# Kernel tuning notes

Measured on AMD Instinct MI355X. Metric: run time of the kernel, lower is better.

Reference implementation:

```python
import jax, jax.numpy as jnp
import numpy as np

NUM_MIRNA = 20000
NUM_GENE = 30000
N = NUM_MIRNA + NUM_GENE  # 50000 homogeneous nodes
R = 4                      # num_relations
E = 1000000                # num edges
IN_C, HID, OUT, NB = 128, 128, 64, 10


def setup_inputs() -> dict:
    key = jax.random.key(0)
    ks = jax.random.split(key, 20)
    s = 0.05
    inp = {}
    inp["x_mirna"] = jax.random.normal(ks[0], (NUM_MIRNA, 256), jnp.float32)
    inp["x_gene"] = jax.random.normal(ks[1], (NUM_GENE, 512), jnp.float32)
    inp["edge_index"] = jax.random.randint(ks[2], (2, E), 0, N)
    inp["edge_type"] = jax.random.randint(ks[3], (E,), 0, R)
    # per-node-type input projections
    inp["lin_w_m"] = jax.random.normal(ks[4], (256, IN_C), jnp.float32) * s
    inp["lin_b_m"] = jnp.zeros((IN_C,), jnp.float32)
    inp["lin_w_g"] = jax.random.normal(ks[5], (512, IN_C), jnp.float32) * s
    inp["lin_b_g"] = jnp.zeros((IN_C,), jnp.float32)
    # RGCNConv layer 1 (basis decomposition)
    inp["comp1"] = jax.random.normal(ks[6], (R, NB), jnp.float32) * s
    inp["basis1"] = jax.random.normal(ks[7], (NB, IN_C, HID), jnp.float32) * s
    inp["root1"] = jax.random.normal(ks[8], (IN_C, HID), jnp.float32) * s
    inp["bias1"] = jnp.zeros((HID,), jnp.float32)
    # RGCNConv layer 2
    inp["comp2"] = jax.random.normal(ks[9], (R, NB), jnp.float32) * s
    inp["basis2"] = jax.random.normal(ks[10], (NB, HID, OUT), jnp.float32) * s
    inp["root2"] = jax.random.normal(ks[11], (HID, OUT), jnp.float32) * s
    inp["bias2"] = jnp.zeros((OUT,), jnp.float32)
    return inp


def rgcn_conv(x, src, dst, etype, comp, basis, root, bias):
    # W_r = sum_b comp[r,b] * basis[b] : [R, I, O]
    W = jnp.einsum('rb,bio->rio', comp, basis)
    # transform every node under every relation: [R, N, O]
    h = jnp.einsum('ni,rio->rno', x, W)
    # gather per-edge message from (relation, source) pair: [E, O]
    msg = h[etype, src]
    # per-(relation, dst) mean aggregation (PyG RGCNConv aggr='mean')
    seg = etype * N + dst
    summed = jax.ops.segment_sum(msg, seg, num_segments=R * N)
    cnt = jax.ops.segment_sum(jnp.ones((msg.shape[0],), msg.dtype), seg,
                              num_segments=R * N)
    mean = summed / jnp.maximum(cnt, 1.0)[:, None]
    agg = mean.reshape(R, N, -1).sum(0)  # sum over relations
    return agg + x @ root + bias


def reference(x_mirna, x_gene, edge_index, edge_type,
              lin_w_m, lin_b_m, lin_w_g, lin_b_g,
              comp1, basis1, root1, bias1,
              comp2, basis2, root2, bias2):
    xm = x_mirna @ lin_w_m + lin_b_m
    xg = x_gene @ lin_w_g + lin_b_g
    x = jnp.concatenate([xm, xg], axis=0)  # to_homogeneous, miRNA first
    src, dst = edge_index[0], edge_index[1]
    x = rgcn_conv(x, src, dst, edge_type, comp1, basis1, root1, bias1)
    x = rgcn_conv(x, src, dst, edge_type, comp2, basis2, root2, bias2)
    return x[:NUM_MIRNA], x[NUM_MIRNA:]
```

## Files before the change

kernel.cpp:

```cpp
#include <hip/hip_runtime.h>
#include <hip/hip_bf16.h>

#define NUM_MIRNA 20000
#define NUM_GENE  30000
#define NN        50000
#define RR        4
#define EE        1000000
#define IN_C      128
#define HIDC      128
#define OUTC      64
#define NBASIS    10
#define NSEG      (RR * NN)
#define NSEGP     200704
#define KFUSE     640
#define SROW      512

#define NBKT   256
#define BSH    8
#define NBKTU  ((NN + 255) >> 8)
#define CHUNK  4096
#define NCHUNK ((EE + CHUNK - 1) / CHUNK)

typedef __attribute__((ext_vector_type(8))) short bf16x8;
typedef __attribute__((ext_vector_type(4))) float f32x4;
typedef __attribute__((ext_vector_type(2))) float f32x2;

__device__ inline ushort f2bf(float x) {
    uint u = __float_as_uint(x);
    uint r = u + 0x7fffu + ((u >> 16) & 1u);
    return (ushort)(r >> 16);
}
__device__ inline float bf2f(ushort b) {
    return __uint_as_float((uint)b << 16);
}
__device__ inline uint pack2bf(float lo, float hi) {
    return (uint)f2bf(lo) | ((uint)f2bf(hi) << 16);
}
__device__ inline f32x2 up2(uint u) {
    return (f32x2){__uint_as_float(u << 16), __uint_as_float(u & 0xffff0000u)};
}

#define GLOAD_LDS16(gsrc, ldst)                                                \
    __builtin_amdgcn_global_load_lds(                                          \
        (const __attribute__((address_space(1))) void*)(gsrc),                 \
        (__attribute__((address_space(3))) void*)(ldst), 16, 0, 0)

__global__ void cvt_k(const float* __restrict__ in, ushort* __restrict__ out, int n4) {
    int i = blockIdx.x * 256 + threadIdx.x;
    if (i >= n4) return;
    float4 v = ((const float4*)in)[i];
    ushort4 o;
    o.x = f2bf(v.x); o.y = f2bf(v.y); o.z = f2bf(v.z); o.w = f2bf(v.w);
    ((ushort4*)out)[i] = o;
}

__global__ void tcast_k(const float* __restrict__ W, ushort* __restrict__ Wt,
                        int K, int OC) {
    int idx = blockIdx.x * 256 + threadIdx.x;
    if (idx >= K * OC) return;
    int o = idx / K, k = idx % K;
    Wt[idx] = f2bf(W[(size_t)k * OC + o]);
}

__global__ void buildW_k(const float* __restrict__ comp, const float* __restrict__ basis,
                         const float* __restrict__ root, ushort* __restrict__ Wt, int O) {
    int idx = blockIdx.x * 256 + threadIdx.x;
    if (idx >= O * KFUSE) return;
    int o = idx / KFUSE, k = idx % KFUSE;
    float acc;
    if (k < 512) {
        int r = k >> 7, i = k & 127;
        acc = 0.f;
#pragma unroll
        for (int b = 0; b < NBASIS; ++b)
            acc += comp[r * NBASIS + b] * basis[((size_t)b * 128 + i) * O + o];
    } else {
        acc = root[(size_t)(k - 512) * O + o];
    }
    Wt[idx] = f2bf(acc);
}

template <int NT, int K, bool OUT_BF16, bool ROOTX>
__global__ __launch_bounds__(256) void sgemm_k(
    const ushort* __restrict__ A, const ushort* __restrict__ xroot,
    const ushort* __restrict__ Wt, const float* __restrict__ bias,
    void* __restrict__ Cout, int M)
{
    constexpr int OC = 2 * NT * 16;
    constexpr int BK = 64;
    constexpr int NTILE = K / BK;
    constexpr int AS = ROOTX ? SROW : K;

    __shared__ __align__(16) ushort As[2 * 4096];

    const int tid  = threadIdx.x;
    const int lane = tid & 63;
    const int wid  = tid >> 6;
    const int wm   = wid >> 1;
    const int wn   = wid & 1;
    const int l15  = lane & 15;
    const int lg   = lane >> 4;
    const int rowBase = blockIdx.x * 64;
    const int colBase = wn * NT * 16;

    f32x4 acc[2][NT];
#pragma unroll
    for (int mt = 0; mt < 2; ++mt)
#pragma unroll
        for (int nt = 0; nt < NT; ++nt)
            acc[mt][nt] = (f32x4){0.f, 0.f, 0.f, 0.f};

    auto STAGE = [&](int buf, int t) {
        const int kc = t * BK;
#pragma unroll
        for (int i = 0; i < 2; ++i) {
            int L   = i * 4096 + tid * 16;
            int row = L >> 7;
            int bs  = (L & 127) ^ ((row & 7) << 4);
            int grow = rowBase + row; if (grow >= M) grow = M - 1;
            const ushort* src;
            if (!ROOTX || kc < SROW)
                src = A + (size_t)grow * AS + kc + (bs >> 1);
            else
                src = xroot + (size_t)grow * IN_C + (kc - SROW) + (bs >> 1);
            GLOAD_LDS16(src, &As[(size_t)buf * 4096 + (L >> 1)]);
        }
    };

    STAGE(0, 0);
    __syncthreads();

#pragma unroll
    for (int t = 0; t < NTILE; ++t) {
        const int kc  = t * BK;
        const int buf = t & 1;

        bf16x8 bB[2][NT];
#pragma unroll
        for (int kk = 0; kk < 2; ++kk)
#pragma unroll
            for (int nt = 0; nt < NT; ++nt)
                bB[kk][nt] = *(const bf16x8*)(
                    Wt + (size_t)(colBase + nt * 16 + l15) * K + kc + kk * 32 + lg * 8);

        if (t + 1 < NTILE) STAGE(buf ^ 1, t + 1);

        bf16x8 aF[2][2];
#pragma unroll
        for (int mt = 0; mt < 2; ++mt)
#pragma unroll
            for (int kk = 0; kk < 2; ++kk) {
                int row = wm * 32 + mt * 16 + l15;
                int kb  = kk * 64 + lg * 16;
                aF[mt][kk] = *(const bf16x8*)&As[
                    (size_t)buf * 4096 + row * 64 + ((kb ^ ((row & 7) << 4)) >> 1)];
            }

#pragma unroll
        for (int kk = 0; kk < 2; ++kk)
#pragma unroll
            for (int nt = 0; nt < NT; ++nt)
#pragma unroll
                for (int mt = 0; mt < 2; ++mt)
                    acc[mt][nt] = __builtin_amdgcn_mfma_f32_16x16x32_bf16(
                        aF[mt][kk], bB[kk][nt], acc[mt][nt], 0, 0, 0);

        __syncthreads();
    }

#pragma unroll
    for (int nt = 0; nt < NT; ++nt) {
        int n = colBase + nt * 16 + l15;
        float bv = bias ? bias[n] : 0.f;
#pragma unroll
        for (int mt = 0; mt < 2; ++mt) {
#pragma unroll
            for (int q = 0; q < 4; ++q) {
                int m = rowBase + wm * 32 + mt * 16 + lg * 4 + q;
                if (m < M) {
                    float v = acc[mt][nt][q] + bv;
                    size_t off = (size_t)m * OC + n;
                    if (OUT_BF16) ((ushort*)Cout)[off] = f2bf(v);
                    else          ((float*)Cout)[off]  = v;
                }
            }
        }
    }
}

__global__ __launch_bounds__(256) void bs0_k(const int* __restrict__ dstA,
                                             int* __restrict__ bcnt) {
    __shared__ int h[NBKT];
    int t = threadIdx.x;
    h[t] = 0;
    __syncthreads();
    int e0 = blockIdx.x * CHUNK;
    int n = EE - e0; if (n > CHUNK) n = CHUNK;
    for (int i = t; i < n; i += 256)
        atomicAdd(&h[dstA[e0 + i] >> BSH], 1);
    __syncthreads();
    if (h[t]) atomicAdd(&bcnt[t], h[t]);
}

__global__ void bscan_k(const int* __restrict__ bcnt, int* __restrict__ bbase,
                        int* __restrict__ bcur) {
    __shared__ int sm[NBKT];
    int t = threadIdx.x;
    int v = bcnt[t];
    sm[t] = v; __syncthreads();
    for (int off = 1; off < NBKT; off <<= 1) {
        int x = (t >= off) ? sm[t - off] : 0;
        __syncthreads();
        sm[t] += x;
        __syncthreads();
    }
    int ex = sm[t] - v;
    bbase[t] = ex;
    bcur[t]  = ex;
}

__global__ __launch_bounds__(256) void bs1_k(const int* __restrict__ srcA,
                                             const int* __restrict__ dstA,
                                             const int* __restrict__ et,
                                             int* __restrict__ bcur,
                                             uint2* __restrict__ bpay) {
    __shared__ int h[NBKT], cur[NBKT], boff[NBKT];
    __shared__ int lseg[CHUNK];
    __shared__ int lsrc[CHUNK];
    int t = threadIdx.x;
    h[t] = 0; cur[t] = 0;
    __syncthreads();
    int e0 = blockIdx.x * CHUNK;
    int n = EE - e0; if (n > CHUNK) n = CHUNK;
    for (int i = t; i < n; i += 256) {
        int e = e0 + i;
        int d = dstA[e];
        int s2 = d * 4 + et[e];
        lseg[i] = s2;
        lsrc[i] = srcA[e];
        atomicAdd(&h[d >> BSH], 1);
    }
    __syncthreads();
    if (h[t]) boff[t] = atomicAdd(&bcur[t], h[t]);
    __syncthreads();
    for (int i = t; i < n; i += 256) {
        int s2 = lseg[i];
        int b = s2 >> (BSH + 2);
        int slot = atomicAdd(&cur[b], 1);
        bpay[boff[b] + slot] = make_uint2((uint)lsrc[i], (uint)s2);
    }
}

__global__ __launch_bounds__(256) void sortbkt_k(
    const uint2* __restrict__ bpay, const int* __restrict__ bbase,
    const int* __restrict__ bcnt, int* __restrict__ sorted,
    int* __restrict__ cnt, int* __restrict__ base, float* __restrict__ inv)
{
    __shared__ int hist[1024];
    __shared__ int tsum[256];
    const int b = blockIdx.x;
    const int t = threadIdx.x;
    const int segbase = b << 10;

#pragma unroll
    for (int i = 0; i < 4; ++i) hist[t + i * 256] = 0;
    __syncthreads();

    const int e0 = bbase[b];
    const int n  = bcnt[b];
    for (int i = t; i < n; i += 256)
        atomicAdd(&hist[(int)bpay[e0 + i].y - segbase], 1);
    __syncthreads();

    int h0 = hist[t * 4], h1 = hist[t * 4 + 1], h2 = hist[t * 4 + 2], h3 = hist[t * 4 + 3];
    int s = h0 + h1 + h2 + h3;
    tsum[t] = s; __syncthreads();
    for (int off = 1; off < 256; off <<= 1) {
        int x = (t >= off) ? tsum[t - off] : 0;
        __syncthreads();
        tsum[t] += x;
        __syncthreads();
    }
    int run = (t > 0) ? tsum[t - 1] : 0;
    int b0 = run, b1 = run + h0, b2 = b1 + h1, b3 = b2 + h2;

    ((int4*)cnt)[(segbase >> 2) + t]  = make_int4(h0, h1, h2, h3);
    ((int4*)base)[(segbase >> 2) + t] = make_int4(e0 + b0, e0 + b1, e0 + b2, e0 + b3);
    ((float4*)inv)[(segbase >> 2) + t] = make_float4(
        1.0f / fmaxf((float)h0, 1.0f), 1.0f / fmaxf((float)h1, 1.0f),
        1.0f / fmaxf((float)h2, 1.0f), 1.0f / fmaxf((float)h3, 1.0f));

    hist[t * 4] = b0; hist[t * 4 + 1] = b1; hist[t * 4 + 2] = b2; hist[t * 4 + 3] = b3;
    __syncthreads();

    for (int i = t; i < n; i += 256) {
        uint2 pr = bpay[e0 + i];
        int pos = atomicAdd(&hist[(int)pr.y - segbase], 1);
        sorted[e0 + pos] = (int)pr.x;
    }
}

__global__ __launch_bounds__(256) void gatherS_k(
    const ushort* __restrict__ x, const int* __restrict__ sorted,
    const int* __restrict__ base, const int* __restrict__ cnt,
    const float* __restrict__ inv, ushort* __restrict__ S)
{
    int d = (blockIdx.x * 256 + threadIdx.x) >> 6;
    int lane = threadIdx.x & 63;
    if (d >= NN) return;
    const uint4* xp = (const uint4*)x;
    uint4* Sp = (uint4*)S;
    const int slot = lane >> 4;
    const int cg   = lane & 15;

    int4   b4 = ((const int4*)base)[d];
    int4   c4 = ((const int4*)cnt)[d];
    float4 w4 = ((const float4*)inv)[d];
    const int off[4]  = {0, b4.y - b4.x, b4.z - b4.x, b4.w - b4.x};
    const int cnts[4] = {c4.x, c4.y, c4.z, c4.w};
    const float wts[4] = {w4.x, w4.y, w4.z, w4.w};
    const int tot = (b4.w + c4.w) - b4.x;

    f32x2 acc[4][4];
#pragma unroll
    for (int r = 0; r < 4; ++r)
#pragma unroll
        for (int t = 0; t < 4; ++t) acc[r][t] = (f32x2){0.f, 0.f};

    if (tot <= 64) {
        int idx = 0;
        if (lane < tot) idx = sorted[b4.x + lane];
        int maxn = max(max(cnts[0], cnts[1]), max(cnts[2], cnts[3]));
        for (int j = 0; j < maxn; j += 4) {
            int e = j + slot;
#pragma unroll
            for (int r = 0; r < 4; ++r) {
                int src = __shfl(idx, off[r] + e);
                if (e < cnts[r]) {
                    uint4 v = xp[(size_t)src * 16 + cg];
                    acc[r][0] += up2(v.x);
                    acc[r][1] += up2(v.y);
                    acc[r][2] += up2(v.z);
                    acc[r][3] += up2(v.w);
                }
            }
        }
    } else {
#pragma unroll
        for (int r = 0; r < 4; ++r) {
            int s0 = b4.x + off[r];
            int s1 = s0 + cnts[r];
            for (int i0 = s0; i0 < s1; i0 += 64) {
                int n = s1 - i0; if (n > 64) n = 64;
                int idx = 0;
                if (lane < n) idx = sorted[i0 + lane];
                for (int j = 0; j < n; j += 4) {
                    int e = j + slot;
                    int src = __shfl(idx, e);
                    if (e < n) {
                        uint4 v = xp[(size_t)src * 16 + cg];
                        acc[r][0] += up2(v.x);
                        acc[r][1] += up2(v.y);
                        acc[r][2] += up2(v.z);
                        acc[r][3] += up2(v.w);
                    }
                }
            }
        }
    }

#pragma unroll
    for (int r = 0; r < 4; ++r) {
        float wt = wts[r];
#pragma unroll
        for (int t = 0; t < 4; ++t) {
            acc[r][t].x += __shfl_xor(acc[r][t].x, 16);
            acc[r][t].y += __shfl_xor(acc[r][t].y, 16);
            acc[r][t].x += __shfl_xor(acc[r][t].x, 32);
            acc[r][t].y += __shfl_xor(acc[r][t].y, 32);
        }
        if (slot == 0) {
            uint4 o;
            o.x = pack2bf(acc[r][0].x * wt, acc[r][0].y * wt);
            o.y = pack2bf(acc[r][1].x * wt, acc[r][1].y * wt);
            o.z = pack2bf(acc[r][2].x * wt, acc[r][2].y * wt);
            o.w = pack2bf(acc[r][3].x * wt, acc[r][3].y * wt);
            Sp[(size_t)d * 64 + r * 16 + cg] = o;
        }
    }
}

extern "C" void kernel_launch(void* const* d_in, const int* in_sizes, int n_in,
                              void* d_out, int out_size, void* d_ws, size_t ws_size,
                              hipStream_t stream) {
    const float* x_mirna = (const float*)d_in[0];
    const float* x_gene  = (const float*)d_in[1];
    const int*   eidx    = (const int*)d_in[2];
    const int*   etype   = (const int*)d_in[3];
    const float* lin_w_m = (const float*)d_in[4];
    const float* lin_b_m = (const float*)d_in[5];
    const float* lin_w_g = (const float*)d_in[6];
    const float* lin_b_g = (const float*)d_in[7];
    const float* comp1   = (const float*)d_in[8];
    const float* basis1  = (const float*)d_in[9];
    const float* root1   = (const float*)d_in[10];
    const float* bias1   = (const float*)d_in[11];
    const float* comp2   = (const float*)d_in[12];
    const float* basis2  = (const float*)d_in[13];
    const float* root2   = (const float*)d_in[14];
    const float* bias2   = (const float*)d_in[15];

    const int* srcA = eidx;
    const int* dstA = eidx + EE;

    char* p = (char*)d_ws;
    ushort* xmbf = (ushort*)p; p += (size_t)NUM_MIRNA * 256 * 2;
    ushort* xgbf = (ushort*)p; p += (size_t)NUM_GENE * 512 * 2;
    ushort* x0bf = (ushort*)p; p += (size_t)NN * IN_C * 2;
    ushort* x1bf = (ushort*)p; p += (size_t)NN * HIDC * 2;
    ushort* S    = (ushort*)p; p += (size_t)NN * SROW * 2;
    ushort* Wtm  = (ushort*)p; p += (size_t)IN_C * 256 * 2;
    ushort* Wtg  = (ushort*)p; p += (size_t)IN_C * 512 * 2;
    ushort* Wt1s = (ushort*)p; p += (size_t)HIDC * KFUSE * 2;
    ushort* Wt2s = (ushort*)p; p += (size_t)OUTC * KFUSE * 2;
    float* inv   = (float*)p;  p += (size_t)NSEGP * 4;
    int* cnt     = (int*)p;    p += (size_t)NSEGP * 4;
    int* base    = (int*)p;    p += (size_t)NSEGP * 4;
    int* bcnt    = (int*)p;    p += NBKT * 4;
    int* bbase   = (int*)p;    p += NBKT * 4;
    int* bcur    = (int*)p;    p += NBKT * 4;
    int* sorted  = (int*)p;    p += (size_t)EE * 4;
    uint2* bpay  = (uint2*)p;  p += (size_t)EE * 8;

    float* outp = (float*)d_out;

    hipMemsetAsync(bcnt, 0, NBKT * sizeof(int), stream);

    cvt_k<<<(NUM_MIRNA * 256 / 4 + 255) / 256, 256, 0, stream>>>(x_mirna, xmbf, NUM_MIRNA * 256 / 4);
    cvt_k<<<(NUM_GENE * 512 / 4 + 255) / 256, 256, 0, stream>>>(x_gene, xgbf, NUM_GENE * 512 / 4);

    tcast_k<<<(256 * IN_C + 255) / 256, 256, 0, stream>>>(lin_w_m, Wtm, 256, IN_C);
    tcast_k<<<(512 * IN_C + 255) / 256, 256, 0, stream>>>(lin_w_g, Wtg, 512, IN_C);
    buildW_k<<<(HIDC * KFUSE + 255) / 256, 256, 0, stream>>>(comp1, basis1, root1, Wt1s, HIDC);
    buildW_k<<<(OUTC * KFUSE + 255) / 256, 256, 0, stream>>>(comp2, basis2, root2, Wt2s, OUTC);

    bs0_k<<<NCHUNK, 256, 0, stream>>>(dstA, bcnt);
    bscan_k<<<1, NBKT, 0, stream>>>(bcnt, bbase, bcur);
    bs1_k<<<NCHUNK, 256, 0, stream>>>(srcA, dstA, etype, bcur, bpay);
    sortbkt_k<<<NBKTU, 256, 0, stream>>>(bpay, bbase, bcnt, sorted, cnt, base, inv);

    sgemm_k<4, 256, true, false><<<dim3((NUM_MIRNA + 63) / 64), 256, 0, stream>>>(
        xmbf, nullptr, Wtm, lin_b_m, x0bf, NUM_MIRNA);
    sgemm_k<4, 512, true, false><<<dim3((NUM_GENE + 63) / 64), 256, 0, stream>>>(
        xgbf, nullptr, Wtg, lin_b_g, x0bf + (size_t)NUM_MIRNA * IN_C, NUM_GENE);

    gatherS_k<<<(NN * 64 + 255) / 256, 256, 0, stream>>>(x0bf, sorted, base, cnt, inv, S);
    sgemm_k<4, KFUSE, true, true><<<dim3((NN + 63) / 64), 256, 0, stream>>>(
        S, x0bf, Wt1s, bias1, x1bf, NN);

    gatherS_k<<<(NN * 64 + 255) / 256, 256, 0, stream>>>(x1bf, sorted, base, cnt, inv, S);
    sgemm_k<2, KFUSE, false, true><<<dim3((NN + 63) / 64), 256, 0, stream>>>(
        S, x1bf, Wt2s, bias2, outp, NN);
}
```

Measured before the change: 287.5 us.

## Pack edge sort payload to 32 bits and make gathers branchless via zero row

```diff
diff --git a/kernel.cpp b/kernel.cpp
--- a/kernel.cpp
+++ b/kernel.cpp
@@ -30,9 +30,6 @@
     uint r = u + 0x7fffu + ((u >> 16) & 1u);
     return (ushort)(r >> 16);
 }
-__device__ inline float bf2f(ushort b) {
-    return __uint_as_float((uint)b << 16);
-}
 __device__ inline uint pack2bf(float lo, float hi) {
     return (uint)f2bf(lo) | ((uint)f2bf(hi) << 16);
 }
@@ -45,13 +42,22 @@
         (const __attribute__((address_space(1))) void*)(gsrc),                 \
         (__attribute__((address_space(3))) void*)(ldst), 16, 0, 0)
 
-__global__ void cvt_k(const float* __restrict__ in, ushort* __restrict__ out, int n4) {
+__global__ void cvt2_k(const float* __restrict__ xm, const float* __restrict__ xg,
+                       ushort* __restrict__ out) {
+    const int n4m = NUM_MIRNA * 256 / 4;
+    const int n4t = n4m + NUM_GENE * 512 / 4;
     int i = blockIdx.x * 256 + threadIdx.x;
-    if (i >= n4) return;
-    float4 v = ((const float4*)in)[i];
+    if (i >= n4t) return;
+    float4 v = (i < n4m) ? ((const float4*)xm)[i] : ((const float4*)xg)[i - n4m];
     ushort4 o;
     o.x = f2bf(v.x); o.y = f2bf(v.y); o.z = f2bf(v.z); o.w = f2bf(v.w);
     ((ushort4*)out)[i] = o;
+}
+
+__global__ void zrow_k(ushort* __restrict__ x0, ushort* __restrict__ x1) {
+    int t = threadIdx.x;
+    if (t < 64)       ((uint*)(x0 + (size_t)NN * 128))[t] = 0u;
+    else if (t < 128) ((uint*)(x1 + (size_t)NN * 128))[t - 64] = 0u;
 }
 
 __global__ void tcast_k(const float* __restrict__ W, ushort* __restrict__ Wt,
@@ -223,10 +229,10 @@
                                              const int* __restrict__ dstA,
                                              const int* __restrict__ et,
                                              int* __restrict__ bcur,
-                                             uint2* __restrict__ bpay) {
+                                             uint* __restrict__ bpay) {
     __shared__ int h[NBKT], cur[NBKT], boff[NBKT];
-    __shared__ int lseg[CHUNK];
-    __shared__ int lsrc[CHUNK];
+    __shared__ uint lpay[CHUNK];
+    __shared__ unsigned char lbkt[CHUNK];
     int t = threadIdx.x;
     h[t] = 0; cur[t] = 0;
     __syncthreads();
@@ -236,23 +242,23 @@
         int e = e0 + i;
         int d = dstA[e];
         int s2 = d * 4 + et[e];
-        lseg[i] = s2;
-        lsrc[i] = srcA[e];
-        atomicAdd(&h[d >> BSH], 1);
+        int b = d >> BSH;
+        lpay[i] = ((uint)(s2 & 1023) << 17) | (uint)srcA[e];
+        lbkt[i] = (unsigned char)b;
+        atomicAdd(&h[b], 1);
     }
     __syncthreads();
     if (h[t]) boff[t] = atomicAdd(&bcur[t], h[t]);
     __syncthreads();
     for (int i = t; i < n; i += 256) {
-        int s2 = lseg[i];
-        int b = s2 >> (BSH + 2);
+        int b = lbkt[i];
         int slot = atomicAdd(&cur[b], 1);
-        bpay[boff[b] + slot] = make_uint2((uint)lsrc[i], (uint)s2);
+        bpay[boff[b] + slot] = lpay[i];
     }
 }
 
 __global__ __launch_bounds__(256) void sortbkt_k(
-    const uint2* __restrict__ bpay, const int* __restrict__ bbase,
+    const uint* __restrict__ bpay, const int* __restrict__ bbase,
     const int* __restrict__ bcnt, int* __restrict__ sorted,
     int* __restrict__ cnt, int* __restrict__ base, float* __restrict__ inv)
 {
@@ -269,7 +275,7 @@
     const int e0 = bbase[b];
     const int n  = bcnt[b];
     for (int i = t; i < n; i += 256)
-        atomicAdd(&hist[(int)bpay[e0 + i].y - segbase], 1);
+        atomicAdd(&hist[(int)(bpay[e0 + i] >> 17)], 1);
     __syncthreads();
 
     int h0 = hist[t * 4], h1 = hist[t * 4 + 1], h2 = hist[t * 4 + 2], h3 = hist[t * 4 + 3];
@@ -294,9 +300,9 @@
     __syncthreads();
 
     for (int i = t; i < n; i += 256) {
-        uint2 pr = bpay[e0 + i];
-        int pos = atomicAdd(&hist[(int)pr.y - segbase], 1);
-        sorted[e0 + pos] = (int)pr.x;
+        uint val = bpay[e0 + i];
+        int pos = atomicAdd(&hist[(int)(val >> 17)], 1);
+        sorted[e0 + pos] = (int)((val & 0x1FFFFu) << 8);
     }
 }
 
@@ -308,15 +314,17 @@
     int d = (blockIdx.x * 256 + threadIdx.x) >> 6;
     int lane = threadIdx.x & 63;
     if (d >= NN) return;
-    const uint4* xp = (const uint4*)x;
+    const char* xb = (const char*)x;
     uint4* Sp = (uint4*)S;
     const int slot = lane >> 4;
     const int cg   = lane & 15;
+    const int cgb  = cg << 4;
+    const int ZB   = NN * 256;
 
     int4   b4 = ((const int4*)base)[d];
     int4   c4 = ((const int4*)cnt)[d];
     float4 w4 = ((const float4*)inv)[d];
-    const int off[4]  = {0, b4.y - b4.x, b4.z - b4.x, b4.w - b4.x};
+    const int ofr[4]  = {0, b4.y - b4.x, b4.z - b4.x, b4.w - b4.x};
     const int cnts[4] = {c4.x, c4.y, c4.z, c4.w};
     const float wts[4] = {w4.x, w4.y, w4.z, w4.w};
     const int tot = (b4.w + c4.w) - b4.x;
@@ -328,42 +336,38 @@
         for (int t = 0; t < 4; ++t) acc[r][t] = (f32x2){0.f, 0.f};
 
     if (tot <= 64) {
-        int idx = 0;
-        if (lane < tot) idx = sorted[b4.x + lane];
+        int idx = sorted[b4.x + lane];
         int maxn = max(max(cnts[0], cnts[1]), max(cnts[2], cnts[3]));
         for (int j = 0; j < maxn; j += 4) {
             int e = j + slot;
 #pragma unroll
             for (int r = 0; r < 4; ++r) {
-                int src = __shfl(idx, off[r] + e);
-                if (e < cnts[r]) {
-                    uint4 v = xp[(size_t)src * 16 + cg];
+                int off = __shfl(idx, ofr[r] + e);
+                off = (e < cnts[r]) ? off : ZB;
+                uint4 v = *(const uint4*)(xb + off + cgb);
+                acc[r][0] += up2(v.x);
+                acc[r][1] += up2(v.y);
+                acc[r][2] += up2(v.z);
+                acc[r][3] += up2(v.w);
+            }
+        }
+    } else {
+#pragma unroll
+        for (int r = 0; r < 4; ++r) {
+            int s0 = b4.x + ofr[r];
+            int s1 = s0 + cnts[r];
+            for (int i0 = s0; i0 < s1; i0 += 64) {
+                int idx2 = sorted[i0 + lane];
+                int n2 = s1 - i0; if (n2 > 64) n2 = 64;
+                for (int j = 0; j < n2; j += 4) {
+                    int e = j + slot;
+                    int off = __shfl(idx2, e);
+                    off = (e < n2) ? off : ZB;
+                    uint4 v = *(const uint4*)(xb + off + cgb);
                     acc[r][0] += up2(v.x);
                     acc[r][1] += up2(v.y);
                     acc[r][2] += up2(v.z);
                     acc[r][3] += up2(v.w);
-                }
-            }
-        }
-    } else {
-#pragma unroll
-        for (int r = 0; r < 4; ++r) {
-            int s0 = b4.x + off[r];
-            int s1 = s0 + cnts[r];
-            for (int i0 = s0; i0 < s1; i0 += 64) {
-                int n = s1 - i0; if (n > 64) n = 64;
-                int idx = 0;
-                if (lane < n) idx = sorted[i0 + lane];
-                for (int j = 0; j < n; j += 4) {
-                    int e = j + slot;
-                    int src = __shfl(idx, e);
-                    if (e < n) {
-                        uint4 v = xp[(size_t)src * 16 + cg];
-                        acc[r][0] += up2(v.x);
-                        acc[r][1] += up2(v.y);
-                        acc[r][2] += up2(v.z);
-                        acc[r][3] += up2(v.w);
-                    }
                 }
             }
         }
@@ -416,8 +420,8 @@
     char* p = (char*)d_ws;
     ushort* xmbf = (ushort*)p; p += (size_t)NUM_MIRNA * 256 * 2;
     ushort* xgbf = (ushort*)p; p += (size_t)NUM_GENE * 512 * 2;
-    ushort* x0bf = (ushort*)p; p += (size_t)NN * IN_C * 2;
-    ushort* x1bf = (ushort*)p; p += (size_t)NN * HIDC * 2;
+    ushort* x0bf = (ushort*)p; p += (size_t)(NN + 1) * IN_C * 2;
+    ushort* x1bf = (ushort*)p; p += (size_t)(NN + 1) * HIDC * 2;
     ushort* S    = (ushort*)p; p += (size_t)NN * SROW * 2;
     ushort* Wtm  = (ushort*)p; p += (size_t)IN_C * 256 * 2;
     ushort* Wtg  = (ushort*)p; p += (size_t)IN_C * 512 * 2;
@@ -429,15 +433,15 @@
     int* bcnt    = (int*)p;    p += NBKT * 4;
     int* bbase   = (int*)p;    p += NBKT * 4;
     int* bcur    = (int*)p;    p += NBKT * 4;
-    int* sorted  = (int*)p;    p += (size_t)EE * 4;
-    uint2* bpay  = (uint2*)p;  p += (size_t)EE * 8;
+    int* sorted  = (int*)p;    p += (size_t)(EE + 64) * 4;
+    uint* bpay   = (uint*)p;   p += (size_t)EE * 4;
 
     float* outp = (float*)d_out;
 
     hipMemsetAsync(bcnt, 0, NBKT * sizeof(int), stream);
 
-    cvt_k<<<(NUM_MIRNA * 256 / 4 + 255) / 256, 256, 0, stream>>>(x_mirna, xmbf, NUM_MIRNA * 256 / 4);
-    cvt_k<<<(NUM_GENE * 512 / 4 + 255) / 256, 256, 0, stream>>>(x_gene, xgbf, NUM_GENE * 512 / 4);
+    cvt2_k<<<(5120000 + 255) / 256, 256, 0, stream>>>(x_mirna, x_gene, xmbf);
+    zrow_k<<<1, 256, 0, stream>>>(x0bf, x1bf);
 
     tcast_k<<<(256 * IN_C + 255) / 256, 256, 0, stream>>>(lin_w_m, Wtm, 256, IN_C);
     tcast_k<<<(512 * IN_C + 255) / 256, 256, 0, stream>>>(lin_w_g, Wtg, 512, IN_C);
```

Result: no change. 291.5 us (+1.4%).
